# Kernel optimization log

Hardware: AMD Instinct MI355X
Metric: run time of the kernel (lower is better)

The kernel has to match this reference:

```python
import jax, jax.numpy as jnp
import numpy as np

TOL = 1e-3


def _image_grads(F):
    # replicate-pad central difference, matches GradientBatch (conv with [-0.5,0,0.5])
    Fx = jnp.pad(F, ((0, 0), (0, 0), (0, 0), (1, 1)), mode='edge')
    gx = 0.5 * (Fx[:, :, :, 2:] - Fx[:, :, :, :-2])
    Fy = jnp.pad(F, ((0, 0), (0, 0), (1, 1), (0, 0)), mode='edge')
    gy = 0.5 * (Fy[:, :, 2:, :] - Fy[:, :, :-2, :])
    return gx, gy


def _param_to_H(p):
    B = p.shape[0]
    z = jnp.zeros((B, 1, 1), p.dtype)
    return jnp.concatenate([p, z], 1).reshape(B, 3, 3) + jnp.eye(3, dtype=p.dtype)


def _bilinear_sample(A, xw, yw):
    # grid_sample(mode='bilinear', align_corners=True, padding_mode='zeros') at pixel coords (xw, yw)
    B, k, h, w = A.shape
    x0 = jnp.floor(xw)
    y0 = jnp.floor(yw)
    fx = (xw - x0).reshape(B, 1, h * w)
    fy = (yw - y0).reshape(B, 1, h * w)
    Af = A.reshape(B, k, h * w)

    def gather(xi, yi):
        valid = (xi >= 0) & (xi <= w - 1) & (yi >= 0) & (yi <= h - 1)
        xi_c = jnp.clip(xi, 0, w - 1).astype(jnp.int32)
        yi_c = jnp.clip(yi, 0, h - 1).astype(jnp.int32)
        idx = (yi_c * w + xi_c).reshape(B, 1, h * w)
        v = jnp.take_along_axis(Af, jnp.broadcast_to(idx, (B, k, h * w)), axis=2)
        return v * valid.reshape(B, 1, h * w).astype(A.dtype)

    v00 = gather(x0, y0)
    v01 = gather(x0 + 1, y0)
    v10 = gather(x0, y0 + 1)
    v11 = gather(x0 + 1, y0 + 1)
    Q = ((1 - fx) * (1 - fy) * v00 + fx * (1 - fy) * v01
         + (1 - fx) * fy * v10 + fx * fy * v11)
    return Q.reshape(B, k, h, w)


def _deeplk(img, temp, init_param, max_itr):
    B, k, h, w = temp.shape
    dt = temp.dtype
    gx, gy = _image_grads(temp)
    # centered pixel grid (meshgrid in source: x - x.max()/2)
    x = jnp.arange(w, dtype=dt) - (w - 1) / 2.0
    y = jnp.arange(h, dtype=dt) - (h - 1) / 2.0
    X, Y = jnp.meshgrid(x, y)  # (h, w); X varies along w
    Xf = jnp.tile(X.reshape(-1), k)  # [k*h*w], tiled per channel
    Yf = jnp.tile(Y.reshape(-1), k)
    gxf = gx.reshape(B, k * h * w)
    gyf = gy.reshape(B, k * h * w)
    dIdp = jnp.stack([
        Xf * gxf, Yf * gxf, gxf,
        Xf * gyf, Yf * gyf, gyf,
        -Xf * Xf * gxf - Xf * Yf * gyf,
        -Xf * Yf * gxf - Yf * Yf * gyf,
    ], axis=2)  # [B, k*h*w, 8]
    Hmat = jnp.einsum('bnp,bnq->bpq', dIdp, dIdp)  # [B,8,8]
    invH = jnp.linalg.inv(Hmat)
    invH_dIdp = jnp.einsum('bpq,bnq->bpn', invH, dIdp)  # [B,8,k*h*w]
    xy = jnp.stack([X.reshape(-1), Y.reshape(-1), jnp.ones((h * w,), dt)], 0)  # [3, h*w]
    tolf = jnp.asarray(TOL, dt)

    def step(carry, _):
        p, dp = carry
        Hm = _param_to_H(p)
        xyw = jnp.einsum('bij,jn->bin', Hm, xy)  # [B,3,h*w]
        Xw = (xyw[:, 0] / xyw[:, 2]).reshape(B, h, w) + (w - 1) / 2.0
        Yw = (xyw[:, 1] / xyw[:, 2]).reshape(B, h, w) + (h - 1) / 2.0
        Fi_warp = _bilinear_sample(img, Xw, Yw)
        xn = Xw / ((w - 1) / 2.0) - 1.0
        yn = Yw / ((h - 1) / 2.0) - 1.0
        mask = ((xn > -1 + 2.0 / w) & (xn < 1 - 2.0 / w)
                & (yn > -1 + 2.0 / h) & (yn < 1 - 2.0 / h)).astype(dt)
        r = (Fi_warp - temp * mask[:, None]).reshape(B, k * h * w, 1)
        dp_new = jnp.einsum('bpn,bnj->bpj', invH_dIdp, r)  # [B,8,1]
        dp_new = dp_new.at[:, 6:8, 0].set(0.0)  # zero projective terms
        active = (jnp.linalg.norm(dp, axis=1, keepdims=True) > tolf).astype(dt)
        dp2 = active * dp_new  # converged samples freeze (dp stays 0)
        return (p - dp2, dp2), None

    dp0 = jnp.ones((B, 8, 1), dt)
    (p, _), _ = jax.lax.scan(step, (init_param, dp0), None, length=max_itr)
    return p


def setup_inputs() -> dict:
    key = jax.random.key(0)
    k1, k2 = jax.random.split(key)
    B, k, h, w = 8, 8, 256, 256
    img = jax.random.normal(k1, (B, k, h, w), dtype=jnp.float32)
    temp = jax.random.normal(k2, (B, k, h, w), dtype=jnp.float32)
    init_param = jnp.zeros((B, 8, 1), dtype=jnp.float32)
    return {"img": img, "temp": temp, "init_param": init_param, "max_itr": 10}


def reference(img, temp, init_param, max_itr):
    p = _deeplk(img, temp, init_param, max_itr)
    return (p, _param_to_H(p))
```

## Files before the change

### kernel.cpp

```cpp
#include <hip/hip_runtime.h>
#include <hip/hip_bf16.h>

#define B_ 8
#define K_ 8
#define H_ 256
#define W_ 256
#define HW (H_*W_)

__device__ __forceinline__ unsigned short f2bf(float f) {
    __hip_bfloat16 h = __float2bfloat16(f);
    return *reinterpret_cast<unsigned short*>(&h);
}
__device__ __forceinline__ void ub8(uint4 u, float* o) {
    o[0] = __uint_as_float(u.x << 16); o[1] = __uint_as_float(u.x & 0xffff0000u);
    o[2] = __uint_as_float(u.y << 16); o[3] = __uint_as_float(u.y & 0xffff0000u);
    o[4] = __uint_as_float(u.z << 16); o[5] = __uint_as_float(u.z & 0xffff0000u);
    o[6] = __uint_as_float(u.w << 16); o[7] = __uint_as_float(u.w & 0xffff0000u);
}
__device__ __forceinline__ float half_reduce(float v) {
    v += __shfl_down(v, 16, 64);
    v += __shfl_down(v, 8, 64);
    v += __shfl_down(v, 4, 64);
    v += __shfl_down(v, 2, 64);
    v += __shfl_down(v, 1, 64);
    return v;
}

__device__ __forceinline__ void pixel_accum(
    const uint4* __restrict__ imgT, const uint4* __restrict__ TG,
    int b, int x, int y,
    float h00, float h01, float h02, float h10, float h11, float h12,
    float h20, float h21, float* aa) {
    const int px = (y << 8) | x;
    const float X = (float)x - 127.5f, Y = (float)y - 127.5f;
    const float zw = h20 * X + h21 * Y + 1.f;
    const float Xw = (h00 * X + h01 * Y + h02) / zw + 127.5f;
    const float Yw = (h10 * X + h11 * Y + h12) / zw + 127.5f;
    const float NLO = -1.f + 2.f / 256.f, NHI = 1.f - 2.f / 256.f;
    const float xn = Xw / 127.5f - 1.f, yn = Yw / 127.5f - 1.f;
    const float m = (xn > NLO && xn < NHI && yn > NLO && yn < NHI) ? 1.f : 0.f;

    const float x0f = floorf(Xw), y0f = floorf(Yw);
    const float fx = Xw - x0f, fy = Yw - y0f;
    const float x1f = x0f + 1.f, y1f = y0f + 1.f;
    const bool vx0 = (x0f >= 0.f) && (x0f <= 255.f);
    const bool vx1 = (x1f >= 0.f) && (x1f <= 255.f);
    const bool vy0 = (y0f >= 0.f) && (y0f <= 255.f);
    const bool vy1 = (y1f >= 0.f) && (y1f <= 255.f);
    const int xi0 = (int)fminf(fmaxf(x0f, 0.f), 255.f);
    const int xi1 = (int)fminf(fmaxf(x1f, 0.f), 255.f);
    const int yi0 = (int)fminf(fmaxf(y0f, 0.f), 255.f);
    const int yi1 = (int)fminf(fmaxf(y1f, 0.f), 255.f);
    const int i00 = yi0 * W_ + xi0, i01 = yi0 * W_ + xi1;
    const int i10 = yi1 * W_ + xi0, i11 = yi1 * W_ + xi1;
    const float w00 = ((vx0 && vy0) ? 1.f : 0.f) * (1.f - fx) * (1.f - fy);
    const float w01 = ((vx1 && vy0) ? 1.f : 0.f) * fx * (1.f - fy);
    const float w10 = ((vx0 && vy1) ? 1.f : 0.f) * (1.f - fx) * fy;
    const float w11 = ((vx1 && vy1) ? 1.f : 0.f) * fx * fy;

    const int base = b * HW;
    const uint4 u00 = imgT[base + i00], u01 = imgT[base + i01];
    const uint4 u10 = imgT[base + i10], u11 = imgT[base + i11];
    const uint4* tg = TG + (size_t)(base + px) * 3;
    const uint4 t0 = tg[0], g0 = tg[1], g1 = tg[2];

    float A00[8], A01[8], A10[8], A11[8], GX[8], GY[8], TV[8];
    ub8(u00, A00); ub8(u01, A01); ub8(u10, A10); ub8(u11, A11);
    ub8(t0, TV);   ub8(g0, GX);   ub8(g1, GY);

    float vx = 0.f, vy = 0.f;
    #pragma unroll
    for (int c = 0; c < 8; ++c) {
        const float Q = w00 * A00[c] + w01 * A01[c] + w10 * A10[c] + w11 * A11[c];
        const float r = Q - TV[c] * m;
        vx += GX[c] * r;
        vy += GY[c] * r;
    }
    const float t0a = X * vx, t4a = Y * vy;
    const float cc = t0a + t4a;
    aa[0] += t0a;      aa[1] += Y * vx;  aa[2] += vx;
    aa[3] += X * vy;   aa[4] += t4a;     aa[5] += vy;
    aa[6] -= X * cc;   aa[7] -= Y * cc;
}

__global__ __launch_bounds__(256) void prep_kernel(
    const float* __restrict__ img, const float* __restrict__ temp,
    uint4* __restrict__ imgT, uint4* __restrict__ TG,
    double* __restrict__ gramP) {
    __shared__ float smem[8192];
    __shared__ float s15[15];
    const int b   = blockIdx.x & 7;
    const int y   = blockIdx.x >> 3;
    const int tid = threadIdx.x;
    const int ym = (y > 0) ? y - 1 : 0;
    const int yp = (y < 255) ? y + 1 : 255;

    #pragma unroll
    for (int j = 0; j < 8; ++j) {
        const int slot = tid + 256 * j;
        const int rowid = slot >> 6, col4 = slot & 63;
        const int c = rowid >> 2, sel = rowid & 3;
        const int sy = (sel == 0) ? ym : ((sel == 2) ? yp : y);
        const float* src = ((sel == 3) ? img : temp)
                         + ((size_t)(b * K_ + c) * HW + sy * W_ + col4 * 4);
        const float4 v = *(const float4*)src;
        *(float4*)&smem[(c * 4 + sel) * 256 + col4 * 4] = v;
    }
    __syncthreads();

    const int x = tid;
    const int px = (y << 8) | x;
    const float X = (float)x - 127.5f, Y = (float)y - 127.5f;
    const int xm = (x > 0) ? x - 1 : 0;
    const int xp = (x < 255) ? x + 1 : 255;
    float Sxx = 0.f, Sxy = 0.f, Syy = 0.f;
    unsigned int imgp[4] = {0, 0, 0, 0};
    unsigned int tgp[12];
    #pragma unroll
    for (int i = 0; i < 12; ++i) tgp[i] = 0u;
    #pragma unroll
    for (int c = 0; c < 8; ++c) {
        const float* R = &smem[c * 1024];
        const float gx = 0.5f * (R[256 + xp] - R[256 + xm]);
        const float gy = 0.5f * (R[512 + x] - R[x]);
        const float tc = R[256 + x];
        const float iv = R[768 + x];
        Sxx += gx * gx; Sxy += gx * gy; Syy += gy * gy;
        const int sh = (c & 1) * 16;
        imgp[c >> 1]     |= ((unsigned int)f2bf(iv)) << sh;
        tgp[c >> 1]      |= ((unsigned int)f2bf(tc)) << sh;
        tgp[4 + (c >> 1)]|= ((unsigned int)f2bf(gx)) << sh;
        tgp[8 + (c >> 1)]|= ((unsigned int)f2bf(gy)) << sh;
    }
    const size_t gpx = (size_t)b * HW + px;
    imgT[gpx] = make_uint4(imgp[0], imgp[1], imgp[2], imgp[3]);
    uint4* tg = TG + gpx * 3;
    tg[0] = make_uint4(tgp[0], tgp[1], tgp[2],  tgp[3]);
    tg[1] = make_uint4(tgp[4], tgp[5], tgp[6],  tgp[7]);
    tg[2] = make_uint4(tgp[8], tgp[9], tgp[10], tgp[11]);
    __syncthreads();

    {
        const float X2 = X * X;
        const float Xp[5] = {1.f, X, X2, X2 * X, X2 * X2};
        #pragma unroll
        for (int n = 0; n < 5; ++n) {
            smem[n * 256 + tid]        = Sxx * Xp[n];
            smem[(5 + n) * 256 + tid]  = Sxy * Xp[n];
            smem[(10 + n) * 256 + tid] = Syy * Xp[n];
        }
    }
    __syncthreads();
    {
        const int e = tid >> 5, l = tid & 31;
        float v = 0.f;
        #pragma unroll
        for (int j = 0; j < 8; ++j) v += smem[e * 256 + l + 32 * j];
        v = half_reduce(v);
        if ((tid & 31) == 0) s15[e] = v;
    }
    if (tid < 224) {
        const int e = 8 + (tid >> 5), l = tid & 31;
        float v = 0.f;
        #pragma unroll
        for (int j = 0; j < 8; ++j) v += smem[e * 256 + l + 32 * j];
        v = half_reduce(v);
        if ((tid & 31) == 0) s15[e] = v;
    }
    __syncthreads();

    if (tid < 36) {
        const int aC[8]  = {1, 1, 1, 0, 0, 0, -1, -1};
        const int aNX[8] = {1, 0, 0, 0, 0, 0,  2,  1};
        const int aNY[8] = {0, 1, 0, 0, 0, 0,  0,  1};
        const int bC[8]  = {0, 0, 0, 1, 1, 1, -1, -1};
        const int bNX[8] = {0, 0, 0, 1, 0, 0,  1,  0};
        const int bNY[8] = {0, 0, 0, 0, 1, 0,  1,  2};
        const double Yd = (double)Y;
        const double Yp2 = Yd * Yd;
        const double Ypw[5] = {1.0, Yd, Yp2, Yp2 * Yd, Yp2 * Yp2};
        int p = 0, rem = tid;
        while (rem >= 8 - p) { rem -= 8 - p; ++p; }
        const int q = p + rem;
        double g = 0.0;
        const int ac = aC[p] * aC[q];
        if (ac) g += ac * Ypw[aNY[p] + aNY[q]] * (double)s15[aNX[p] + aNX[q]];
        const int ab1 = aC[p] * bC[q];
        if (ab1) g += ab1 * Ypw[aNY[p] + bNY[q]] * (double)s15[5 + aNX[p] + bNX[q]];
        const int ab2 = bC[p] * aC[q];
        if (ab2) g += ab2 * Ypw[bNY[p] + aNY[q]] * (double)s15[5 + bNX[p] + aNX[q]];
        const int bc = bC[p] * bC[q];
        if (bc) g += bc * Ypw[bNY[p] + bNY[q]] * (double)s15[10 + bNX[p] + bNX[q]];
        gramP[((size_t)b * 36 + tid) * 256 + y] = g;
    }
}

__global__ __launch_bounds__(256) void iter_kernel(
    const uint4* __restrict__ imgT, const uint4* __restrict__ TG,
    const double* __restrict__ gramP, double* __restrict__ invHg,
    const double* __restrict__ invH, const float* __restrict__ init_param,
    const double* __restrict__ stateR, double* __restrict__ stateW,
    const float* __restrict__ sPrev, float* __restrict__ sNext,
    const int* __restrict__ max_itr, int iter) {
    if (iter >= *max_itr) return;
    __shared__ float red[2048];
    __shared__ float s8[8];
    __shared__ double sh_invH[64];
    __shared__ double sh_st[16];
    __shared__ double sh_pd[16];
    const int tid = threadIdx.x;

    if (iter == 0 && blockIdx.x >= 512) {
        const int b = blockIdx.x - 512;
        __shared__ double gpart[144];
        __shared__ double shA[64];
        __shared__ double shB[64];
        if (tid < 144) {
            const int e = tid >> 2, q = tid & 3;
            const double* gp = gramP + ((size_t)b * 36 + e) * 256 + q * 64;
            double acc = 0.0;
            #pragma unroll 8
            for (int i = 0; i < 64; ++i) acc += gp[i];
            gpart[tid] = acc;
        }
        __syncthreads();
        const int i = tid >> 3, j = tid & 7;
        if (tid < 64) {
            const int pp = min(i, j), qq = max(i, j);
            const int tri = 8 * pp - (pp * (pp - 1)) / 2 + (qq - pp);
            shA[tid] = gpart[tri * 4] + gpart[tri * 4 + 1]
                     + gpart[tri * 4 + 2] + gpart[tri * 4 + 3];
            shB[tid] = (i == j) ? 1.0 : 0.0;
        }
        __syncthreads();
        for (int k = 0; k < 8; ++k) {
            const double piv = shA[k * 8 + k];
            __syncthreads();
            if (tid < 64 && i == k) { shA[tid] /= piv; shB[tid] /= piv; }
            __syncthreads();
            double f = 0, ak = 0, bk = 0;
            if (tid < 64) { f = shA[i * 8 + k]; ak = shA[k * 8 + j]; bk = shB[k * 8 + j]; }
            __syncthreads();
            if (tid < 64 && i != k) { shA[tid] -= f * ak; shB[tid] -= f * bk; }
            __syncthreads();
        }
        if (tid < 64) invHg[b * 64 + tid] = shB[tid];
        return;
    }

    const int b   = blockIdx.x & 7;
    const int yb  = blockIdx.x >> 3;

    if (iter > 0) {
        if (tid < 64) sh_invH[tid] = invH[b * 64 + tid];
        if (tid >= 64 && tid < 72) sh_st[tid - 64] = stateR[b * 8 + (tid - 64)];
        if (tid >= 72 && tid < 80) sh_st[tid - 64] = stateR[64 + b * 8 + (tid - 72)];
    }

    if (iter == 0) {
        if (tid < 8) {
            sh_pd[tid]     = (double)init_param[b * 8 + tid];
            sh_pd[8 + tid] = 1.0;
        }
        __syncthreads();
    } else {
        const float* sR = sPrev + b * 512;
        const int e = tid >> 5, l = tid & 31;
        float v = sR[e * 64 + l] + sR[e * 64 + 32 + l];
        v = half_reduce(v);
        if ((tid & 31) == 0) s8[tid >> 5] = v;
        __syncthreads();
        if (tid < 8) {
            double nrm2 = 0.0;
            #pragma unroll
            for (int k2 = 0; k2 < 8; ++k2) {
                const double d = sh_st[8 + k2];
                nrm2 += d * d;
            }
            double dpn = 0.0;
            if (tid < 6) {
                #pragma unroll
                for (int k2 = 0; k2 < 8; ++k2)
                    dpn += sh_invH[tid * 8 + k2] * (double)s8[k2];
            }
            const double dp2 = (sqrt(nrm2) > 1e-3) ? dpn : 0.0;
            sh_pd[tid]     = sh_st[tid] - dp2;
            sh_pd[8 + tid] = dp2;
        }
        __syncthreads();
    }
    if (yb == 0 && tid < 8) {
        stateW[b * 8 + tid]      = sh_pd[tid];
        stateW[64 + b * 8 + tid] = sh_pd[8 + tid];
    }

    const float h00 = 1.f + (float)sh_pd[0], h01 = (float)sh_pd[1], h02 = (float)sh_pd[2];
    const float h10 = (float)sh_pd[3], h11 = 1.f + (float)sh_pd[4], h12 = (float)sh_pd[5];
    const float h20 = (float)sh_pd[6], h21 = (float)sh_pd[7];

    float aa[8];
    #pragma unroll
    for (int e = 0; e < 8; ++e) aa[e] = 0.f;
    #pragma unroll 1
    for (int sub = 0; sub < 4; ++sub) {
        pixel_accum(imgT, TG, b, tid, yb * 4 + sub,
                    h00, h01, h02, h10, h11, h12, h20, h21, aa);
    }

    #pragma unroll
    for (int e = 0; e < 8; ++e) red[e * 256 + tid] = aa[e];
    __syncthreads();
    {
        const int e = tid >> 5, l = tid & 31;
        float v = 0.f;
        #pragma unroll
        for (int j = 0; j < 8; ++j) v += red[e * 256 + l + 32 * j];
        v = half_reduce(v);
        if ((tid & 31) == 0) sNext[b * 512 + e * 64 + yb] = v;
    }
}

__global__ void output_kernel(const double* __restrict__ invH,
                              const float* __restrict__ init_param,
                              const double* __restrict__ st0,
                              const double* __restrict__ st1,
                              const float* __restrict__ sP0,
                              const float* __restrict__ sP1,
                              const int* __restrict__ max_itr,
                              float* __restrict__ out) {
    const int b   = blockIdx.x;
    const int tid = threadIdx.x;
    const int mi_raw = *max_itr;
    const int mi = (mi_raw > 10) ? 10 : mi_raw;
    if (mi <= 0) {
        if (tid < 8) out[b * 8 + tid] = init_param[b * 8 + tid];
        if (tid < 9) {
            float v = (tid < 8) ? init_param[b * 8 + tid] : 0.f;
            if (tid == 0 || tid == 4 || tid == 8) v += 1.f;
            out[64 + b * 9 + tid] = v;
        }
        return;
    }
    const int pr = (mi - 1) & 1;
    const double* st = pr ? st1 : st0;
    const float*  sP = pr ? sP1 : sP0;
    __shared__ float s8[8];
    __shared__ float sh_pf[8];
    const float* sb = sP + b * 512;
    const int e = tid >> 5, l = tid & 31;
    float v = sb[e * 64 + l] + sb[e * 64 + 32 + l];
    v = half_reduce(v);
    if ((tid & 31) == 0) s8[tid >> 5] = v;
    __syncthreads();
    if (tid < 8) {
        double nrm2 = 0.0;
        #pragma unroll
        for (int k2 = 0; k2 < 8; ++k2) {
            const double d = st[64 + b * 8 + k2];
            nrm2 += d * d;
        }
        double dpn = 0.0;
        if (tid < 6) {
            #pragma unroll
            for (int k2 = 0; k2 < 8; ++k2)
                dpn += invH[b * 64 + tid * 8 + k2] * (double)s8[k2];
        }
        const double dp2 = (sqrt(nrm2) > 1e-3) ? dpn : 0.0;
        const float pf = (float)(st[b * 8 + tid] - dp2);
        sh_pf[tid] = pf;
        out[b * 8 + tid] = pf;
    }
    __syncthreads();
    if (tid < 9) {
        float v2 = (tid < 8) ? sh_pf[tid] : 0.f;
        if (tid == 0 || tid == 4 || tid == 8) v2 += 1.f;
        out[64 + b * 9 + tid] = v2;
    }
}

extern "C" void kernel_launch(void* const* d_in, const int* in_sizes, int n_in,
                              void* d_out, int out_size, void* d_ws, size_t ws_size,
                              hipStream_t stream) {
    const float* img        = (const float*)d_in[0];
    const float* temp       = (const float*)d_in[1];
    const float* init_param = (const float*)d_in[2];
    const int*   max_itr    = (const int*)d_in[3];
    float* out = (float*)d_out;

    char* w = (char*)d_ws;
    double* gramP = (double*)w;
    double* st0   = gramP + 73728;
    double* st1   = st0 + 128;
    double* invH  = st1 + 128;
    float*  sP0   = (float*)(invH + 512);
    float*  sP1   = sP0 + 4096;
    uint4* imgT   = (uint4*)(w + 1048576);
    uint4* TG     = (uint4*)(w + 1048576 + 8388608);

    prep_kernel<<<B_ * H_, 256, 0, stream>>>(img, temp, imgT, TG, gramP);
    for (int it = 0; it < 10; ++it) {
        const double* stR = (it & 1) ? st0 : st1;
        double*       stW = (it & 1) ? st1 : st0;
        const float*  sR  = (it & 1) ? sP0 : sP1;
        float*        sW  = (it & 1) ? sP1 : sP0;
        const int grid = (it == 0) ? 520 : 512;
        iter_kernel<<<grid, 256, 0, stream>>>(imgT, TG, gramP, invH, invH,
                                              init_param, stR, stW, sR, sW,
                                              max_itr, it);
    }
    output_kernel<<<B_, 256, 0, stream>>>(invH, init_param, st0, st1,
                                          sP0, sP1, max_itr, out);
}
```

Baseline: 164.4 us.

## Fuse per-iteration kernels into one persistent cooperative kernel with per-batch barriers

Replaces the ten per-iteration launches and the output kernel with a single persistent cooperative kernel. Blocks of the same batch synchronise through per-batch atomic counters instead of kernel boundaries, and the template and gradient data stay cached in shared memory across iterations. The inverse-Hessian solve is folded into iteration 0 of the yb==0 block. This removes launch overhead and repeated global loads but adds spin-wait latency, larger LDS use that may lower occupancy, and reliance on all blocks being co-resident.

New measurement: 535.9 us. 226% more time.

```diff
diff --git a/kernel.cpp b/kernel.cpp
--- a/kernel.cpp
+++ b/kernel.cpp
@@ -26,12 +26,17 @@
     return v;
 }
 
+__device__ __forceinline__ void wait_count(unsigned int* p, unsigned int target) {
+    while (__hip_atomic_load(p, __ATOMIC_RELAXED, __HIP_MEMORY_SCOPE_AGENT) < target)
+        __builtin_amdgcn_s_sleep(8);
+}
+
 __device__ __forceinline__ void pixel_accum(
-    const uint4* __restrict__ imgT, const uint4* __restrict__ TG,
+    const uint4* __restrict__ imgT,
+    const uint4 t0, const uint4 g0, const uint4 g1,
     int b, int x, int y,
     float h00, float h01, float h02, float h10, float h11, float h12,
     float h20, float h21, float* aa) {
-    const int px = (y << 8) | x;
     const float X = (float)x - 127.5f, Y = (float)y - 127.5f;
     const float zw = h20 * X + h21 * Y + 1.f;
     const float Xw = (h00 * X + h01 * Y + h02) / zw + 127.5f;
@@ -61,20 +66,18 @@
     const int base = b * HW;
     const uint4 u00 = imgT[base + i00], u01 = imgT[base + i01];
     const uint4 u10 = imgT[base + i10], u11 = imgT[base + i11];
-    const uint4* tg = TG + (size_t)(base + px) * 3;
-    const uint4 t0 = tg[0], g0 = tg[1], g1 = tg[2];
-
-    float A00[8], A01[8], A10[8], A11[8], GX[8], GY[8], TV[8];
+
+    float A00[8], A01[8], A10[8], A11[8], GXa[8], GYa[8], TV[8];
     ub8(u00, A00); ub8(u01, A01); ub8(u10, A10); ub8(u11, A11);
-    ub8(t0, TV);   ub8(g0, GX);   ub8(g1, GY);
+    ub8(t0, TV);   ub8(g0, GXa);  ub8(g1, GYa);
 
     float vx = 0.f, vy = 0.f;
     #pragma unroll
     for (int c = 0; c < 8; ++c) {
         const float Q = w00 * A00[c] + w01 * A01[c] + w10 * A10[c] + w11 * A11[c];
         const float r = Q - TV[c] * m;
-        vx += GX[c] * r;
-        vy += GY[c] * r;
+        vx += GXa[c] * r;
+        vy += GYa[c] * r;
     }
     const float t0a = X * vx, t4a = Y * vy;
     const float cc = t0a + t4a;
@@ -86,12 +89,16 @@
 __global__ __launch_bounds__(256) void prep_kernel(
     const float* __restrict__ img, const float* __restrict__ temp,
     uint4* __restrict__ imgT, uint4* __restrict__ TG,
-    double* __restrict__ gramP) {
+    double* __restrict__ gramP, unsigned int* __restrict__ bar) {
     __shared__ float smem[8192];
     __shared__ float s15[15];
     const int b   = blockIdx.x & 7;
     const int y   = blockIdx.x >> 3;
     const int tid = threadIdx.x;
+
+    if (blockIdx.x < 8 && tid < 16)
+        bar[(blockIdx.x * 16 + tid) * 32] = 0u;
+
     const int ym = (y > 0) ? y - 1 : 0;
     const int yp = (y < 255) ? y + 1 : 255;
 
@@ -195,143 +202,150 @@
     }
 }
 
-__global__ __launch_bounds__(256) void iter_kernel(
+__global__ __launch_bounds__(256, 2) void fused_kernel(
     const uint4* __restrict__ imgT, const uint4* __restrict__ TG,
     const double* __restrict__ gramP, double* __restrict__ invHg,
-    const double* __restrict__ invH, const float* __restrict__ init_param,
-    const double* __restrict__ stateR, double* __restrict__ stateW,
-    const float* __restrict__ sPrev, float* __restrict__ sNext,
-    const int* __restrict__ max_itr, int iter) {
-    if (iter >= *max_itr) return;
+    const float* __restrict__ init_param,
+    float* __restrict__ sP0, float* __restrict__ sP1,
+    unsigned int* __restrict__ bar,
+    const int* __restrict__ max_itr, float* __restrict__ out) {
+    __shared__ uint4 sT[1024], sGX[1024], sGY[1024];
     __shared__ float red[2048];
     __shared__ float s8[8];
     __shared__ double sh_invH[64];
-    __shared__ double sh_st[16];
     __shared__ double sh_pd[16];
+    __shared__ float sh_pf[8];
+    __shared__ double gpart[144];
+    __shared__ double shA[64], shB[64];
+
     const int tid = threadIdx.x;
-
-    if (iter == 0 && blockIdx.x >= 512) {
-        const int b = blockIdx.x - 512;
-        __shared__ double gpart[144];
-        __shared__ double shA[64];
-        __shared__ double shB[64];
-        if (tid < 144) {
-            const int e = tid >> 2, q = tid & 3;
-            const double* gp = gramP + ((size_t)b * 36 + e) * 256 + q * 64;
-            double acc = 0.0;
-            #pragma unroll 8
-            for (int i = 0; i < 64; ++i) acc += gp[i];
-            gpart[tid] = acc;
-        }
-        __syncthreads();
-        const int i = tid >> 3, j = tid & 7;
-        if (tid < 64) {
-            const int pp = min(i, j), qq = max(i, j);
-            const int tri = 8 * pp - (pp * (pp - 1)) / 2 + (qq - pp);
-            shA[tid] = gpart[tri * 4] + gpart[tri * 4 + 1]
-                     + gpart[tri * 4 + 2] + gpart[tri * 4 + 3];
-            shB[tid] = (i == j) ? 1.0 : 0.0;
-        }
-        __syncthreads();
-        for (int k = 0; k < 8; ++k) {
-            const double piv = shA[k * 8 + k];
-            __syncthreads();
-            if (tid < 64 && i == k) { shA[tid] /= piv; shB[tid] /= piv; }
-            __syncthreads();
-            double f = 0, ak = 0, bk = 0;
-            if (tid < 64) { f = shA[i * 8 + k]; ak = shA[k * 8 + j]; bk = shB[k * 8 + j]; }
-            __syncthreads();
-            if (tid < 64 && i != k) { shA[tid] -= f * ak; shB[tid] -= f * bk; }
-            __syncthreads();
-        }
-        if (tid < 64) invHg[b * 64 + tid] = shB[tid];
-        return;
-    }
-
     const int b   = blockIdx.x & 7;
     const int yb  = blockIdx.x >> 3;
-
-    if (iter > 0) {
-        if (tid < 64) sh_invH[tid] = invH[b * 64 + tid];
-        if (tid >= 64 && tid < 72) sh_st[tid - 64] = stateR[b * 8 + (tid - 64)];
-        if (tid >= 72 && tid < 80) sh_st[tid - 64] = stateR[64 + b * 8 + (tid - 72)];
-    }
-
-    if (iter == 0) {
-        if (tid < 8) {
-            sh_pd[tid]     = (double)init_param[b * 8 + tid];
-            sh_pd[8 + tid] = 1.0;
-        }
-        __syncthreads();
-    } else {
-        const float* sR = sPrev + b * 512;
-        const int e = tid >> 5, l = tid & 31;
-        float v = sR[e * 64 + l] + sR[e * 64 + 32 + l];
-        v = half_reduce(v);
-        if ((tid & 31) == 0) s8[tid >> 5] = v;
-        __syncthreads();
-        if (tid < 8) {
-            double nrm2 = 0.0;
-            #pragma unroll
-            for (int k2 = 0; k2 < 8; ++k2) {
-                const double d = sh_st[8 + k2];
-                nrm2 += d * d;
-            }
-            double dpn = 0.0;
-            if (tid < 6) {
-                #pragma unroll
-                for (int k2 = 0; k2 < 8; ++k2)
-                    dpn += sh_invH[tid * 8 + k2] * (double)s8[k2];
-            }
-            const double dp2 = (sqrt(nrm2) > 1e-3) ? dpn : 0.0;
-            sh_pd[tid]     = sh_st[tid] - dp2;
-            sh_pd[8 + tid] = dp2;
-        }
-        __syncthreads();
-    }
-    if (yb == 0 && tid < 8) {
-        stateW[b * 8 + tid]      = sh_pd[tid];
-        stateW[64 + b * 8 + tid] = sh_pd[8 + tid];
-    }
-
-    const float h00 = 1.f + (float)sh_pd[0], h01 = (float)sh_pd[1], h02 = (float)sh_pd[2];
-    const float h10 = (float)sh_pd[3], h11 = 1.f + (float)sh_pd[4], h12 = (float)sh_pd[5];
-    const float h20 = (float)sh_pd[6], h21 = (float)sh_pd[7];
-
-    float aa[8];
-    #pragma unroll
-    for (int e = 0; e < 8; ++e) aa[e] = 0.f;
-    #pragma unroll 1
-    for (int sub = 0; sub < 4; ++sub) {
-        pixel_accum(imgT, TG, b, tid, yb * 4 + sub,
-                    h00, h01, h02, h10, h11, h12, h20, h21, aa);
-    }
-
-    #pragma unroll
-    for (int e = 0; e < 8; ++e) red[e * 256 + tid] = aa[e];
-    __syncthreads();
-    {
-        const int e = tid >> 5, l = tid & 31;
-        float v = 0.f;
-        #pragma unroll
-        for (int j = 0; j < 8; ++j) v += red[e * 256 + l + 32 * j];
-        v = half_reduce(v);
-        if ((tid & 31) == 0) sNext[b * 512 + e * 64 + yb] = v;
-    }
-}
-
-__global__ void output_kernel(const double* __restrict__ invH,
-                              const float* __restrict__ init_param,
-                              const double* __restrict__ st0,
-                              const double* __restrict__ st1,
-                              const float* __restrict__ sP0,
-                              const float* __restrict__ sP1,
-                              const int* __restrict__ max_itr,
-                              float* __restrict__ out) {
-    const int b   = blockIdx.x;
-    const int tid = threadIdx.x;
     const int mi_raw = *max_itr;
     const int mi = (mi_raw > 10) ? 10 : mi_raw;
+
+    {
+        const size_t base = (size_t)b * HW + (size_t)yb * 1024;
+        #pragma unroll
+        for (int sub = 0; sub < 4; ++sub) {
+            const int pxl = sub * 256 + tid;
+            const uint4* tg = TG + (base + pxl) * 3;
+            sT[pxl] = tg[0]; sGX[pxl] = tg[1]; sGY[pxl] = tg[2];
+        }
+    }
+    __syncthreads();
+
+    for (int it = 0; it < mi; ++it) {
+        if (it > 0) {
+            if (tid == 0) wait_count(&bar[(b * 16 + (it - 1)) * 32], 64u);
+            __syncthreads();
+            __builtin_amdgcn_fence(__ATOMIC_ACQUIRE, "agent");
+            if (it == 1 && tid < 64) sh_invH[tid] = invHg[b * 64 + tid];
+
+            const float* sR = ((it & 1) ? sP0 : sP1) + b * 512;
+            const int e = tid >> 5, l = tid & 31;
+            float v = sR[e * 64 + l] + sR[e * 64 + 32 + l];
+            v = half_reduce(v);
+            if ((tid & 31) == 0) s8[tid >> 5] = v;
+            __syncthreads();
+            if (tid < 8) {
+                double nrm2 = 0.0;
+                #pragma unroll
+                for (int k2 = 0; k2 < 8; ++k2) {
+                    const double d = sh_pd[8 + k2];
+                    nrm2 += d * d;
+                }
+                double dpn = 0.0;
+                if (tid < 6) {
+                    #pragma unroll
+                    for (int k2 = 0; k2 < 8; ++k2)
+                        dpn += sh_invH[tid * 8 + k2] * (double)s8[k2];
+                }
+                const double dp2 = (sqrt(nrm2) > 1e-3) ? dpn : 0.0;
+                const double pnew = sh_pd[tid] - dp2;
+                sh_pd[tid]     = pnew;
+                sh_pd[8 + tid] = dp2;
+            }
+            __syncthreads();
+        } else {
+            if (tid < 8) {
+                sh_pd[tid]     = (double)init_param[b * 8 + tid];
+                sh_pd[8 + tid] = 1.0;
+            }
+            __syncthreads();
+        }
+
+        const float h00 = 1.f + (float)sh_pd[0], h01 = (float)sh_pd[1], h02 = (float)sh_pd[2];
+        const float h10 = (float)sh_pd[3], h11 = 1.f + (float)sh_pd[4], h12 = (float)sh_pd[5];
+        const float h20 = (float)sh_pd[6], h21 = (float)sh_pd[7];
+
+        float aa[8];
+        #pragma unroll
+        for (int e = 0; e < 8; ++e) aa[e] = 0.f;
+        #pragma unroll 1
+        for (int sub = 0; sub < 4; ++sub) {
+            const int pxl = sub * 256 + tid;
+            pixel_accum(imgT, sT[pxl], sGX[pxl], sGY[pxl], b, tid, yb * 4 + sub,
+                        h00, h01, h02, h10, h11, h12, h20, h21, aa);
+        }
+
+        #pragma unroll
+        for (int e = 0; e < 8; ++e) red[e * 256 + tid] = aa[e];
+        __syncthreads();
+        {
+            const int e = tid >> 5, l = tid & 31;
+            float v = 0.f;
+            #pragma unroll
+            for (int j = 0; j < 8; ++j) v += red[e * 256 + l + 32 * j];
+            v = half_reduce(v);
+            if ((tid & 31) == 0) {
+                float* sW = (it & 1) ? sP1 : sP0;
+                sW[b * 512 + e * 64 + yb] = v;
+            }
+        }
+
+        if (it == 0 && yb == 0) {
+            if (tid < 144) {
+                const int e = tid >> 2, q = tid & 3;
+                const double* gp = gramP + ((size_t)b * 36 + e) * 256 + q * 64;
+                double acc = 0.0;
+                #pragma unroll 8
+                for (int i = 0; i < 64; ++i) acc += gp[i];
+                gpart[tid] = acc;
+            }
+            __syncthreads();
+            const int i = tid >> 3, j = tid & 7;
+            if (tid < 64) {
+                const int pp = min(i, j), qq = max(i, j);
+                const int tri = 8 * pp - (pp * (pp - 1)) / 2 + (qq - pp);
+                shA[tid] = gpart[tri * 4] + gpart[tri * 4 + 1]
+                         + gpart[tri * 4 + 2] + gpart[tri * 4 + 3];
+                shB[tid] = (i == j) ? 1.0 : 0.0;
+            }
+            __syncthreads();
+            for (int k = 0; k < 8; ++k) {
+                const double piv = shA[k * 8 + k];
+                __syncthreads();
+                if (tid < 64 && i == k) { shA[tid] /= piv; shB[tid] /= piv; }
+                __syncthreads();
+                double f = 0, ak = 0, bk = 0;
+                if (tid < 64) { f = shA[i * 8 + k]; ak = shA[k * 8 + j]; bk = shB[k * 8 + j]; }
+                __syncthreads();
+                if (tid < 64 && i != k) { shA[tid] -= f * ak; shB[tid] -= f * bk; }
+                __syncthreads();
+            }
+            if (tid < 64) invHg[b * 64 + tid] = shB[tid];
+        }
+
+        __syncthreads();
+        if (tid == 0) {
+            __threadfence();
+            __hip_atomic_fetch_add(&bar[(b * 16 + it) * 32], 1u,
+                                   __ATOMIC_RELEASE, __HIP_MEMORY_SCOPE_AGENT);
+        }
+    }
+
+    if (yb != 0) return;
     if (mi <= 0) {
         if (tid < 8) out[b * 8 + tid] = init_param[b * 8 + tid];
         if (tid < 9) {
@@ -341,32 +355,32 @@
         }
         return;
     }
-    const int pr = (mi - 1) & 1;
-    const double* st = pr ? st1 : st0;
-    const float*  sP = pr ? sP1 : sP0;
-    __shared__ float s8[8];
-    __shared__ float sh_pf[8];
-    const float* sb = sP + b * 512;
-    const int e = tid >> 5, l = tid & 31;
-    float v = sb[e * 64 + l] + sb[e * 64 + 32 + l];
-    v = half_reduce(v);
-    if ((tid & 31) == 0) s8[tid >> 5] = v;
+    if (tid == 0) wait_count(&bar[(b * 16 + (mi - 1)) * 32], 64u);
+    __syncthreads();
+    __builtin_amdgcn_fence(__ATOMIC_ACQUIRE, "agent");
+    {
+        const float* sb = (((mi - 1) & 1) ? sP1 : sP0) + b * 512;
+        const int e = tid >> 5, l = tid & 31;
+        float v = sb[e * 64 + l] + sb[e * 64 + 32 + l];
+        v = half_reduce(v);
+        if ((tid & 31) == 0) s8[tid >> 5] = v;
+    }
     __syncthreads();
     if (tid < 8) {
         double nrm2 = 0.0;
         #pragma unroll
         for (int k2 = 0; k2 < 8; ++k2) {
-            const double d = st[64 + b * 8 + k2];
+            const double d = sh_pd[8 + k2];
             nrm2 += d * d;
         }
         double dpn = 0.0;
         if (tid < 6) {
             #pragma unroll
             for (int k2 = 0; k2 < 8; ++k2)
-                dpn += invH[b * 64 + tid * 8 + k2] * (double)s8[k2];
+                dpn += invHg[b * 64 + tid * 8 + k2] * (double)s8[k2];
         }
         const double dp2 = (sqrt(nrm2) > 1e-3) ? dpn : 0.0;
-        const float pf = (float)(st[b * 8 + tid] - dp2);
+        const float pf = (float)(sh_pd[tid] - dp2);
         sh_pf[tid] = pf;
         out[b * 8 + tid] = pf;
     }
@@ -389,25 +403,23 @@
 
     char* w = (char*)d_ws;
     double* gramP = (double*)w;
-    double* st0   = gramP + 73728;
-    double* st1   = st0 + 128;
-    double* invH  = st1 + 128;
+    double* invH  = gramP + 73728;
     float*  sP0   = (float*)(invH + 512);
     float*  sP1   = sP0 + 4096;
+    unsigned int* bar = (unsigned int*)(sP1 + 4096);
     uint4* imgT   = (uint4*)(w + 1048576);
     uint4* TG     = (uint4*)(w + 1048576 + 8388608);
 
-    prep_kernel<<<B_ * H_, 256, 0, stream>>>(img, temp, imgT, TG, gramP);
-    for (int it = 0; it < 10; ++it) {
-        const double* stR = (it & 1) ? st0 : st1;
-        double*       stW = (it & 1) ? st1 : st0;
-        const float*  sR  = (it & 1) ? sP0 : sP1;
-        float*        sW  = (it & 1) ? sP1 : sP0;
-        const int grid = (it == 0) ? 520 : 512;
-        iter_kernel<<<grid, 256, 0, stream>>>(imgT, TG, gramP, invH, invH,
-                                              init_param, stR, stW, sR, sW,
-                                              max_itr, it);
-    }
-    output_kernel<<<B_, 256, 0, stream>>>(invH, init_param, st0, st1,
-                                          sP0, sP1, max_itr, out);
-}
+    prep_kernel<<<B_ * H_, 256, 0, stream>>>(img, temp, imgT, TG, gramP, bar);
+
+    void* args[] = {(void*)&imgT, (void*)&TG, (void*)&gramP, (void*)&invH,
+                    (void*)&init_param, (void*)&sP0, (void*)&sP1, (void*)&bar,
+                    (void*)&max_itr, (void*)&out};
+    hipError_t err = hipLaunchCooperativeKernel((void*)fused_kernel,
+                                                dim3(512), dim3(256),
+                                                args, 0, stream);
+    if (err != hipSuccess) {
+        fused_kernel<<<512, 256, 0, stream>>>(imgT, TG, gramP, invH, init_param,
+                                              sP0, sP1, bar, max_itr, out);
+    }
+}
```

## Split template/gradient arrays into planar buffers and use one row per block

Applied to the files above, without the earlier changes.

The interleaved template/gx/gy buffer is split into three separate planar arrays, so each thread's loads of a given component are contiguous across the warp. The iteration kernel now processes one image row per block instead of four, which quadruples the grid to 2048 blocks and enlarges the partial-sum buffers to match. The bf16 unpack now extracts values inline instead of going through temporary arrays. More blocks should hide gather latency better, at the cost of more partial sums for the next iteration and the output kernel to reduce, and more per-block setup work such as the invH loads.

Result: no change. 161.4 us (-1.9%).

```diff
diff --git a/kernel.cpp b/kernel.cpp
--- a/kernel.cpp
+++ b/kernel.cpp
@@ -11,11 +11,9 @@
     __hip_bfloat16 h = __float2bfloat16(f);
     return *reinterpret_cast<unsigned short*>(&h);
 }
-__device__ __forceinline__ void ub8(uint4 u, float* o) {
-    o[0] = __uint_as_float(u.x << 16); o[1] = __uint_as_float(u.x & 0xffff0000u);
-    o[2] = __uint_as_float(u.y << 16); o[3] = __uint_as_float(u.y & 0xffff0000u);
-    o[4] = __uint_as_float(u.z << 16); o[5] = __uint_as_float(u.z & 0xffff0000u);
-    o[6] = __uint_as_float(u.w << 16); o[7] = __uint_as_float(u.w & 0xffff0000u);
+__device__ __forceinline__ float bfex(uint4 u, int c) {
+    const unsigned int w = (&u.x)[c >> 1];
+    return __uint_as_float((c & 1) ? (w & 0xffff0000u) : (w << 16));
 }
 __device__ __forceinline__ float half_reduce(float v) {
     v += __shfl_down(v, 16, 64);
@@ -27,11 +25,11 @@
 }
 
 __device__ __forceinline__ void pixel_accum(
-    const uint4* __restrict__ imgT, const uint4* __restrict__ TG,
+    const uint4* __restrict__ imgT,
+    const uint4 t0, const uint4 g0, const uint4 g1,
     int b, int x, int y,
     float h00, float h01, float h02, float h10, float h11, float h12,
     float h20, float h21, float* aa) {
-    const int px = (y << 8) | x;
     const float X = (float)x - 127.5f, Y = (float)y - 127.5f;
     const float zw = h20 * X + h21 * Y + 1.f;
     const float Xw = (h00 * X + h01 * Y + h02) / zw + 127.5f;
@@ -61,20 +59,15 @@
     const int base = b * HW;
     const uint4 u00 = imgT[base + i00], u01 = imgT[base + i01];
     const uint4 u10 = imgT[base + i10], u11 = imgT[base + i11];
-    const uint4* tg = TG + (size_t)(base + px) * 3;
-    const uint4 t0 = tg[0], g0 = tg[1], g1 = tg[2];
-
-    float A00[8], A01[8], A10[8], A11[8], GX[8], GY[8], TV[8];
-    ub8(u00, A00); ub8(u01, A01); ub8(u10, A10); ub8(u11, A11);
-    ub8(t0, TV);   ub8(g0, GX);   ub8(g1, GY);
 
     float vx = 0.f, vy = 0.f;
     #pragma unroll
     for (int c = 0; c < 8; ++c) {
-        const float Q = w00 * A00[c] + w01 * A01[c] + w10 * A10[c] + w11 * A11[c];
-        const float r = Q - TV[c] * m;
-        vx += GX[c] * r;
-        vy += GY[c] * r;
+        const float Q = w00 * bfex(u00, c) + w01 * bfex(u01, c)
+                      + w10 * bfex(u10, c) + w11 * bfex(u11, c);
+        const float r = Q - bfex(t0, c) * m;
+        vx += bfex(g0, c) * r;
+        vy += bfex(g1, c) * r;
     }
     const float t0a = X * vx, t4a = Y * vy;
     const float cc = t0a + t4a;
@@ -85,7 +78,8 @@
 
 __global__ __launch_bounds__(256) void prep_kernel(
     const float* __restrict__ img, const float* __restrict__ temp,
-    uint4* __restrict__ imgT, uint4* __restrict__ TG,
+    uint4* __restrict__ imgT, uint4* __restrict__ TGt,
+    uint4* __restrict__ TGx, uint4* __restrict__ TGy,
     double* __restrict__ gramP) {
     __shared__ float smem[8192];
     __shared__ float s15[15];
@@ -134,10 +128,9 @@
     }
     const size_t gpx = (size_t)b * HW + px;
     imgT[gpx] = make_uint4(imgp[0], imgp[1], imgp[2], imgp[3]);
-    uint4* tg = TG + gpx * 3;
-    tg[0] = make_uint4(tgp[0], tgp[1], tgp[2],  tgp[3]);
-    tg[1] = make_uint4(tgp[4], tgp[5], tgp[6],  tgp[7]);
-    tg[2] = make_uint4(tgp[8], tgp[9], tgp[10], tgp[11]);
+    TGt[gpx] = make_uint4(tgp[0], tgp[1], tgp[2],  tgp[3]);
+    TGx[gpx] = make_uint4(tgp[4], tgp[5], tgp[6],  tgp[7]);
+    TGy[gpx] = make_uint4(tgp[8], tgp[9], tgp[10], tgp[11]);
     __syncthreads();
 
     {
@@ -157,7 +150,7 @@
         #pragma unroll
         for (int j = 0; j < 8; ++j) v += smem[e * 256 + l + 32 * j];
         v = half_reduce(v);
-        if ((tid & 31) == 0) s15[e] = v;
+        if (l == 0) s15[e] = v;
     }
     if (tid < 224) {
         const int e = 8 + (tid >> 5), l = tid & 31;
@@ -196,7 +189,8 @@
 }
 
 __global__ __launch_bounds__(256) void iter_kernel(
-    const uint4* __restrict__ imgT, const uint4* __restrict__ TG,
+    const uint4* __restrict__ imgT, const uint4* __restrict__ TGt,
+    const uint4* __restrict__ TGx, const uint4* __restrict__ TGy,
     const double* __restrict__ gramP, double* __restrict__ invHg,
     const double* __restrict__ invH, const float* __restrict__ init_param,
     const double* __restrict__ stateR, double* __restrict__ stateW,
@@ -206,12 +200,12 @@
     __shared__ float red[2048];
     __shared__ float s8[8];
     __shared__ double sh_invH[64];
-    __shared__ double sh_st[16];
     __shared__ double sh_pd[16];
+
     const int tid = threadIdx.x;
 
-    if (iter == 0 && blockIdx.x >= 512) {
-        const int b = blockIdx.x - 512;
+    if (iter == 0 && blockIdx.x >= 2048) {
+        const int b = blockIdx.x - 2048;
         __shared__ double gpart[144];
         __shared__ double shA[64];
         __shared__ double shB[64];
@@ -248,14 +242,8 @@
         return;
     }
 
-    const int b   = blockIdx.x & 7;
-    const int yb  = blockIdx.x >> 3;
-
-    if (iter > 0) {
-        if (tid < 64) sh_invH[tid] = invH[b * 64 + tid];
-        if (tid >= 64 && tid < 72) sh_st[tid - 64] = stateR[b * 8 + (tid - 64)];
-        if (tid >= 72 && tid < 80) sh_st[tid - 64] = stateR[64 + b * 8 + (tid - 72)];
-    }
+    const int b  = blockIdx.x & 7;
+    const int yb = blockIdx.x >> 3;
 
     if (iter == 0) {
         if (tid < 8) {
@@ -264,17 +252,22 @@
         }
         __syncthreads();
     } else {
-        const float* sR = sPrev + b * 512;
-        const int e = tid >> 5, l = tid & 31;
-        float v = sR[e * 64 + l] + sR[e * 64 + 32 + l];
-        v = half_reduce(v);
-        if ((tid & 31) == 0) s8[tid >> 5] = v;
+        if (tid < 64) sh_invH[tid] = invH[b * 64 + tid];
+        {
+            const float* sR = sPrev + b * 2048;
+            const int e = tid >> 5, l = tid & 31;
+            float v = 0.f;
+            #pragma unroll
+            for (int j = 0; j < 8; ++j) v += sR[e * 256 + l + 32 * j];
+            v = half_reduce(v);
+            if (l == 0) s8[e] = v;
+        }
         __syncthreads();
         if (tid < 8) {
             double nrm2 = 0.0;
             #pragma unroll
             for (int k2 = 0; k2 < 8; ++k2) {
-                const double d = sh_st[8 + k2];
+                const double d = stateR[64 + b * 8 + k2];
                 nrm2 += d * d;
             }
             double dpn = 0.0;
@@ -284,7 +277,7 @@
                     dpn += sh_invH[tid * 8 + k2] * (double)s8[k2];
             }
             const double dp2 = (sqrt(nrm2) > 1e-3) ? dpn : 0.0;
-            sh_pd[tid]     = sh_st[tid] - dp2;
+            sh_pd[tid]     = stateR[b * 8 + tid] - dp2;
             sh_pd[8 + tid] = dp2;
         }
         __syncthreads();
@@ -301,9 +294,10 @@
     float aa[8];
     #pragma unroll
     for (int e = 0; e < 8; ++e) aa[e] = 0.f;
-    #pragma unroll 1
-    for (int sub = 0; sub < 4; ++sub) {
-        pixel_accum(imgT, TG, b, tid, yb * 4 + sub,
+    {
+        const size_t gpx = (size_t)b * HW + (size_t)yb * W_ + tid;
+        const uint4 t0 = TGt[gpx], g0 = TGx[gpx], g1 = TGy[gpx];
+        pixel_accum(imgT, t0, g0, g1, b, tid, yb,
                     h00, h01, h02, h10, h11, h12, h20, h21, aa);
     }
 
@@ -316,7 +310,7 @@
         #pragma unroll
         for (int j = 0; j < 8; ++j) v += red[e * 256 + l + 32 * j];
         v = half_reduce(v);
-        if ((tid & 31) == 0) sNext[b * 512 + e * 64 + yb] = v;
+        if (l == 0) sNext[b * 2048 + e * 256 + yb] = v;
     }
 }
 
@@ -346,11 +340,15 @@
     const float*  sP = pr ? sP1 : sP0;
     __shared__ float s8[8];
     __shared__ float sh_pf[8];
-    const float* sb = sP + b * 512;
-    const int e = tid >> 5, l = tid & 31;
-    float v = sb[e * 64 + l] + sb[e * 64 + 32 + l];
-    v = half_reduce(v);
-    if ((tid & 31) == 0) s8[tid >> 5] = v;
+    {
+        const float* sb = sP + b * 2048;
+        const int e = tid >> 5, l = tid & 31;
+        float v = 0.f;
+        #pragma unroll
+        for (int j = 0; j < 8; ++j) v += sb[e * 256 + l + 32 * j];
+        v = half_reduce(v);
+        if (l == 0) s8[e] = v;
+    }
     __syncthreads();
     if (tid < 8) {
         double nrm2 = 0.0;
@@ -393,20 +391,23 @@
     double* st1   = st0 + 128;
     double* invH  = st1 + 128;
     float*  sP0   = (float*)(invH + 512);
-    float*  sP1   = sP0 + 4096;
+    float*  sP1   = sP0 + 16384;
     uint4* imgT   = (uint4*)(w + 1048576);
-    uint4* TG     = (uint4*)(w + 1048576 + 8388608);
-
-    prep_kernel<<<B_ * H_, 256, 0, stream>>>(img, temp, imgT, TG, gramP);
+    uint4* TGt    = (uint4*)(w + 1048576 + 8388608);
+    uint4* TGx    = TGt + (size_t)B_ * HW;
+    uint4* TGy    = TGx + (size_t)B_ * HW;
+
+    prep_kernel<<<B_ * H_, 256, 0, stream>>>(img, temp, imgT, TGt, TGx, TGy,
+                                             gramP);
     for (int it = 0; it < 10; ++it) {
         const double* stR = (it & 1) ? st0 : st1;
         double*       stW = (it & 1) ? st1 : st0;
         const float*  sR  = (it & 1) ? sP0 : sP1;
         float*        sW  = (it & 1) ? sP1 : sP0;
-        const int grid = (it == 0) ? 520 : 512;
-        iter_kernel<<<grid, 256, 0, stream>>>(imgT, TG, gramP, invH, invH,
-                                              init_param, stR, stW, sR, sW,
-                                              max_itr, it);
+        const int grid = (it == 0) ? 2056 : 2048;
+        iter_kernel<<<grid, 256, 0, stream>>>(imgT, TGt, TGx, TGy, gramP,
+                                              invH, invH, init_param,
+                                              stR, stW, sR, sW, max_itr, it);
     }
     output_kernel<<<B_, 256, 0, stream>>>(invH, init_param, st0, st1,
                                           sP0, sP1, max_itr, out);
```
